# Performance work log

Hardware: AMD Instinct MI355X
Metric: run time of the kernel (lower is better)

## Reference

```python
import jax, jax.numpy as jnp
import numpy as np

H, L, P, D_MODEL = 8, 4, 4, 256
HD = D_MODEL // H
SPATIAL = np.array([[100, 100], [50, 50], [25, 25], [13, 13]], dtype=np.int64)  # (h, w) per level


def _bilinear_sample(feat, gx, gy, lh, lw):
    """Bilinear sampling matching torch.F.grid_sample(align_corners=False, padding_mode='zeros').
    feat: [BH, lh*lw, D]; gx, gy: [BH, Nq, P] pixel coords. Returns [BH, Nq, P, D]."""
    x0 = jnp.floor(gx); y0 = jnp.floor(gy)
    wx = gx - x0; wy = gy - y0

    def gather(xf, yf):
        xi = xf.astype(jnp.int32); yi = yf.astype(jnp.int32)
        valid = (xi >= 0) & (xi < lw) & (yi >= 0) & (yi < lh)
        idx = jnp.clip(yi, 0, lh - 1) * lw + jnp.clip(xi, 0, lw - 1)
        BH = feat.shape[0]
        v = jnp.take_along_axis(feat, idx.reshape(BH, -1)[:, :, None], axis=1)
        v = v.reshape(xi.shape + (feat.shape[-1],))
        return v * valid[..., None].astype(feat.dtype)

    return (gather(x0, y0) * ((1 - wx) * (1 - wy))[..., None]
            + gather(x0 + 1, y0) * (wx * (1 - wy))[..., None]
            + gather(x0, y0 + 1) * ((1 - wx) * wy)[..., None]
            + gather(x0 + 1, y0 + 1) * (wx * wy)[..., None])


def _msda(query, reference_points, value, sp_np, Wso, bso, Waw, baw, Wv, bv, Wo, bo):
    B, Nq, _ = query.shape
    Nv = value.shape[1]
    v = (value @ Wv + bv).reshape(B, Nv, H, HD)  # value_proj
    off = (query @ Wso + bso).reshape(B, Nq, H, L, P, 2)  # sampling_offsets
    wh = jnp.asarray(sp_np[:, ::-1].copy(), jnp.float32)  # (w, h) per level
    loc = reference_points[:, :, None, :, None, :] + off / wh[None, None, None, :, None, :]
    grid = 2.0 * loc - 1.0  # [B, Nq, H, L, P, 2] in [-1, 1]
    aw = jax.nn.softmax((query @ Waw + baw).reshape(B, Nq, H, L * P), axis=-1).reshape(B, Nq, H, L, P)
    starts = np.concatenate([[0], np.cumsum(sp_np[:, 0] * sp_np[:, 1])]).astype(np.int64)
    out = jnp.zeros((B, H, Nq, HD), dtype=query.dtype)
    for lid in range(L):
        lh, lw = int(sp_np[lid, 0]), int(sp_np[lid, 1])
        feat = v[:, starts[lid]:starts[lid + 1]].transpose(0, 2, 1, 3).reshape(B * H, lh * lw, HD)
        g = grid[:, :, :, lid].transpose(0, 2, 1, 3, 4).reshape(B * H, Nq, P, 2)
        # align_corners=False: x_pix = ((gx + 1) * W - 1) / 2
        gx = (g[..., 0] + 1.0) * (lw * 0.5) - 0.5
        gy = (g[..., 1] + 1.0) * (lh * 0.5) - 0.5
        samp = _bilinear_sample(feat, gx, gy, lh, lw)  # [B*H, Nq, P, HD]
        w_l = aw[:, :, :, lid].transpose(0, 2, 1, 3).reshape(B * H, Nq, P)
        out = out + (samp * w_l[..., None]).sum(axis=2).reshape(B, H, Nq, HD)
    out = out.transpose(0, 2, 1, 3).reshape(B, Nq, D_MODEL)
    return out @ Wo + bo  # output_proj


def setup_inputs() -> dict:
    key = jax.random.key(0)
    ks = jax.random.split(key, 12)
    B, Nq = 2, int(np.sum(SPATIAL[:, 0] * SPATIAL[:, 1]))  # encoder: Nq == Nv == 13294
    Nv = Nq
    s = 1.0 / np.sqrt(D_MODEL).astype(np.float32)
    return {
        "query": jax.random.normal(ks[0], (B, Nq, D_MODEL), jnp.float32),
        "reference_points": jax.random.uniform(ks[1], (B, Nq, L, 2), dtype=jnp.float32),
        "value": jax.random.normal(ks[2], (B, Nv, D_MODEL), jnp.float32),
        "spatial_shapes": jnp.asarray(SPATIAL),
        "Wso": jax.random.normal(ks[3], (D_MODEL, H * L * P * 2), jnp.float32) * 0.01,
        "bso": jax.random.normal(ks[4], (H * L * P * 2,), jnp.float32) * 0.5,
        "Waw": jax.random.normal(ks[5], (D_MODEL, H * L * P), jnp.float32) * 0.01,
        "baw": jnp.zeros((H * L * P,), jnp.float32),
        "Wv": jax.random.normal(ks[6], (D_MODEL, D_MODEL), jnp.float32) * s,
        "bv": jnp.zeros((D_MODEL,), jnp.float32),
        "Wo": jax.random.normal(ks[7], (D_MODEL, D_MODEL), jnp.float32) * s,
        "bo": jnp.zeros((D_MODEL,), jnp.float32),
    }


def reference(query, reference_points, value, spatial_shapes, Wso, bso, Waw, baw, Wv, bv, Wo, bo):
    sp_np = np.asarray(spatial_shapes)  # static level shapes
    return _msda(query, reference_points, value, sp_np, Wso, bso, Waw, baw, Wv, bv, Wo, bo)
```

## Files before the change

### kernel.cpp

```cpp
#include <hip/hip_runtime.h>
#include <hip/hip_bf16.h>
#include <hip/hip_fp16.h>

typedef short s16x8 __attribute__((ext_vector_type(8)));
typedef float f32x4 __attribute__((ext_vector_type(4)));
typedef unsigned int u32x4 __attribute__((ext_vector_type(4)));
typedef unsigned int u32x2 __attribute__((ext_vector_type(2)));

constexpr int Bb = 2, NQ = 13294, Hh = 8, HD = 32;
constexpr int Mrows = Bb * NQ;

__device__ inline short bf16_of(float f) {
  __hip_bfloat16 h = __float2bfloat16(f);
  return *reinterpret_cast<short*>(&h);
}

__device__ __forceinline__ void gload16(const void* g, void* l) {
  __builtin_amdgcn_global_load_lds(
      (const __attribute__((address_space(1))) unsigned int*)g,
      (__attribute__((address_space(3))) unsigned int*)l, 16, 0, 0);
}

__global__ __launch_bounds__(256) void prep_k(
    const float* __restrict__ Wv, const float* __restrict__ Wso,
    const float* __restrict__ Waw, const float* __restrict__ Wo,
    const float* __restrict__ bso, const float* __restrict__ baw,
    short* __restrict__ WvT, short* __restrict__ WqT, short* __restrict__ WoT,
    float* __restrict__ bq)
{
  __shared__ short lds[64][65];
  const int tid = threadIdx.x;
  int t = blockIdx.x;
  if (t == 56) {
#pragma unroll
    for (int i = 0; i < 2; i++) {
      int id = i * 256 + tid;
      if (id < 384) bq[id] = id < 256 ? bso[id] : baw[id - 256];
    }
    return;
  }
  const float* src; short* dst; int ldS, n0, k0, drow0;
  if (t < 16)      { src = Wv;  dst = WvT; ldS = 256; n0 = (t >> 2) * 64;        k0 = (t & 3) * 64; drow0 = n0; }
  else if (t < 32) { t -= 16; src = Wso; dst = WqT; ldS = 256; n0 = (t >> 2) * 64; k0 = (t & 3) * 64; drow0 = n0; }
  else if (t < 40) { t -= 32; src = Waw; dst = WqT; ldS = 128; n0 = (t >> 2) * 64; k0 = (t & 3) * 64; drow0 = 256 + n0; }
  else             { t -= 40; src = Wo;  dst = WoT; ldS = 256; n0 = (t >> 2) * 64; k0 = (t & 3) * 64; drow0 = n0; }

#pragma unroll
  for (int i = 0; i < 16; i++) {
    int idx = i * 256 + tid;
    int kk = idx >> 6, nn = idx & 63;
    lds[nn][kk] = bf16_of(src[(size_t)(k0 + kk) * ldS + n0 + nn]);
  }
  __syncthreads();
#pragma unroll
  for (int i = 0; i < 16; i++) {
    int idx = i * 256 + tid;
    int nn = idx >> 6, kk = idx & 63;
    dst[(size_t)(drow0 + nn) * 256 + k0 + kk] = lds[nn][kk];
  }
}

template<int MODE>
__device__ __forceinline__ void gemm_body(
    const void* __restrict__ Araw, const short* __restrict__ WT,
    const float* __restrict__ bias, void* __restrict__ outraw,
    int wg, char* __restrict__ ldsA, char* __restrict__ ldsB)
{
  constexpr int NT = (MODE == 1) ? 6 : 4;
  constexpr int ABYTES = (MODE == 3) ? 8192 : 16384;
  const int xcd = wg & 7, local = wg >> 3;
  const int row0 = (xcd * 26 + local / NT) * 128;
  const int col0 = (local % NT) * 64;
  const int tid = threadIdx.x, lane = tid & 63, wave = tid >> 6;
  const int fr = lane & 15, kg = lane >> 4;

  float bvf[4];
#pragma unroll
  for (int n = 0; n < 4; n++) bvf[n] = bias[col0 + n * 16 + fr];
  asm volatile("" :: "v"(bvf[0]), "v"(bvf[1]), "v"(bvf[2]), "v"(bvf[3]));

  const int rowB = tid >> 2, slB = (tid & 3) ^ (rowB & 3);
  const short* srcB = WT + (size_t)(col0 + rowB) * 256 + slB * 8;
  const int ldoffB = tid * 16;

  const float* srcAf[4]; const short* srcAs[2]; int ldoffA[4];
  if constexpr (MODE == 3) {
#pragma unroll
    for (int i = 0; i < 2; i++) {
      int rowA = i * 64 + (tid >> 2);
      int rowc = min(row0 + rowA, Mrows - 1);
      int slA = (tid & 3) ^ (rowA & 3);
      srcAs[i] = (const short*)Araw + (size_t)rowc * 256 + slA * 8;
      ldoffA[i] = i * 4096 + tid * 16;
    }
  } else {
#pragma unroll
    for (int i = 0; i < 4; i++) {
      int rowA = i * 32 + (tid >> 3);
      int rowc = min(row0 + rowA, Mrows - 1);
      int slA = (tid & 7) ^ (rowA & 7);
      srcAf[i] = (const float*)Araw + (size_t)rowc * 256 + slA * 4;
      ldoffA[i] = i * 4096 + tid * 16;
    }
  }

  auto stage = [&](int bufsel, int kt) {
    char* Ab = ldsA + bufsel * ABYTES;
    char* Bd = ldsB + bufsel * 4096;
    if constexpr (MODE == 3) {
#pragma unroll
      for (int i = 0; i < 2; i++) gload16(srcAs[i] + kt, Ab + ldoffA[i]);
    } else {
#pragma unroll
      for (int i = 0; i < 4; i++) gload16(srcAf[i] + kt, Ab + ldoffA[i]);
    }
    gload16(srcB + kt, Bd + ldoffB);
  };

  f32x4 acc[2][4] = {};
  stage(0, 0);

#pragma unroll
  for (int t = 0; t < 8; t++) {
    const int buf = t & 1;
    if (t < 7) {
      stage(buf ^ 1, (t + 1) * 32);
      if constexpr (MODE == 3) asm volatile("s_waitcnt vmcnt(3)" ::: "memory");
      else                     asm volatile("s_waitcnt vmcnt(5)" ::: "memory");
    } else {
      asm volatile("s_waitcnt vmcnt(0)" ::: "memory");
    }
    __builtin_amdgcn_s_barrier();

    const char* Ab = ldsA + buf * ABYTES;
    const char* Bd = ldsB + buf * 4096;
    s16x8 afr[2], bfr[4];
#pragma unroll
    for (int m = 0; m < 2; m++) {
      const int row = wave * 32 + m * 16 + fr;
      if constexpr (MODE == 3) {
        const int slot = kg ^ (row & 3);
        afr[m] = *(const s16x8*)(Ab + row * 64 + slot * 16);
      } else {
        const int s0 = (2 * kg) ^ (row & 7);
        const f32x4 lo = *(const f32x4*)(Ab + row * 128 + s0 * 16);
        const f32x4 hi = *(const f32x4*)(Ab + row * 128 + (s0 ^ 1) * 16);
        s16x8 av;
#pragma unroll
        for (int i = 0; i < 4; i++) { av[i] = bf16_of(lo[i]); av[4 + i] = bf16_of(hi[i]); }
        afr[m] = av;
      }
    }
#pragma unroll
    for (int n = 0; n < 4; n++) {
      const int row = n * 16 + fr;
      const int slot = kg ^ (row & 3);
      bfr[n] = *(const s16x8*)(Bd + row * 64 + slot * 16);
    }
    asm volatile("s_waitcnt lgkmcnt(0)" ::: "memory");
    __builtin_amdgcn_s_barrier();

#pragma unroll
    for (int m = 0; m < 2; m++)
#pragma unroll
      for (int n = 0; n < 4; n++)
        acc[m][n] = __builtin_amdgcn_mfma_f32_16x16x32_bf16(afr[m], bfr[n], acc[m][n], 0, 0, 0);
  }

#pragma unroll
  for (int n = 0; n < 4; n++) {
    const int colL = col0 + n * 16 + fr;
#pragma unroll
    for (int m = 0; m < 2; m++) {
#pragma unroll
      for (int r = 0; r < 4; r++) {
        const int rowL = row0 + wave * 32 + m * 16 + kg * 4 + r;
        if (rowL < Mrows) {
          float v = acc[m][n][r] + bvf[n];
          if constexpr (MODE == 0) {
            int b = rowL >= NQ, nn = rowL - b * NQ;
            int h = colL >> 5, c = colL & 31;
            ((__half*)outraw)[(((size_t)b * Hh + h) * NQ + nn) * HD + c] = __float2half(v);
          } else if constexpr (MODE == 1) {
            ((__hip_bfloat16*)outraw)[(size_t)rowL * 384 + colL] = __float2bfloat16(v);
          } else {
            ((float*)outraw)[(size_t)rowL * 256 + colL] = v;
          }
        }
      }
    }
  }
}

__global__ __launch_bounds__(256) void gemm01_k(
    const float* __restrict__ value, const float* __restrict__ query,
    const short* __restrict__ WvT, const short* __restrict__ WqT,
    const float* __restrict__ bv, const float* __restrict__ bq,
    __half* __restrict__ vproj, __hip_bfloat16* __restrict__ offaw)
{
  __shared__ __align__(16) char lds[40960];
  char* ldsA = lds;
  char* ldsB = lds + 32768;
  const int wg = blockIdx.x;
  if (wg < 832) gemm_body<0>(value, WvT, bv, vproj, wg, ldsA, ldsB);
  else          gemm_body<1>(query, WqT, bq, offaw, wg - 832, ldsA, ldsB);
}

__global__ __launch_bounds__(256) void gemm3_k(
    const short* __restrict__ interm, const short* __restrict__ WoT,
    const float* __restrict__ bo, float* __restrict__ out)
{
  __shared__ __align__(16) char lds[24576];
  char* ldsA = lds;
  char* ldsB = lds + 16384;
  gemm_body<3>(interm, WoT, bo, out, blockIdx.x, ldsA, ldsB);
}

__global__ __launch_bounds__(256, 8) void sample_k(
    const __half* __restrict__ vproj,
    const __hip_bfloat16* __restrict__ offaw,
    const float* __restrict__ refp,
    __hip_bfloat16* __restrict__ interm)
{
  __shared__ u32x2 dpk[16][2][65];
  const int plane = blockIdx.x & 15;
  const int chunk = blockIdx.x >> 4;
  const int b = plane >> 3, h = plane & 7;
  const int q0 = chunk * 64;
  const int tid = threadIdx.x;
  const int wv = tid >> 6, lane = tid & 63;
  const int dims[4]   = {100, 50, 25, 13};
  const int starts[4] = {0, 10000, 12500, 13125};

#pragma unroll
  for (int it = 0; it < 4; it++) {
    const int ql = wv * 16 + it * 4 + (lane >> 4);
    const int lp = lane & 15;
    const int l = lp >> 2;
    const int lw = dims[l];
    int q = q0 + ql; if (q >= NQ) q = NQ - 1;
    const size_t row = (size_t)b * NQ + q;
    unsigned int oxy = *(const unsigned int*)((const unsigned short*)offaw + row * 384 + h * 32 + lp * 2);
    float offx = __uint_as_float(oxy << 16);
    float offy = __uint_as_float(oxy & 0xffff0000u);
    float logit = __bfloat162float(offaw[row * 384 + 256 + h * 16 + lp]);
    float2 rp = *(const float2*)(refp + (row * 4 + l) * 2);
    float gx = rp.x * (float)lw + offx - 0.5f;
    float gy = rp.y * (float)lw + offy - 0.5f;
    float e = __expf(logit);
    float ssum = e;
#pragma unroll
    for (int d = 1; d < 16; d <<= 1) ssum += __shfl_xor(ssum, d);
    float aw = e / ssum;

    float xf = floorf(gx), yf = floorf(gy);
    int x0 = (int)xf, y0 = (int)yf;
    float wx = gx - xf, wy = gy - yf;
    int bx = min(max(x0, 0), lw - 2);
    bool lxv = (x0 >= 0) & (x0 < lw);
    bool rxv = (x0 + 1 >= 0) & (x0 + 1 < lw);
    float wl = 1.f - wx, wr = wx;
    float ws0 = (lxv && x0 == bx     ? wl : 0.f) + (rxv && x0 + 1 == bx     ? wr : 0.f);
    float ws1 = (lxv && x0 == bx + 1 ? wl : 0.f) + (rxv && x0 + 1 == bx + 1 ? wr : 0.f);
    const int pbase = (b * Hh + h) * NQ + starts[l];
#pragma unroll
    for (int yi = 0; yi < 2; yi++) {
      int yc = y0 + yi;
      bool yv = (yc >= 0) & (yc < lw);
      int ycl = min(max(yc, 0), lw - 1);
      float wyt = (yi ? wy : 1.f - wy) * aw * (yv ? 1.f : 0.f);
      __half h0 = __float2half(ws0 * wyt);
      __half h1 = __float2half(ws1 * wyt);
      u32x2 pk;
      pk[0] = (unsigned int)((pbase + ycl * lw + bx) << 6);
      pk[1] = (unsigned int)(*(unsigned short*)&h0)
            | ((unsigned int)(*(unsigned short*)&h1) << 16);
      dpk[lp][yi][ql] = pk;
    }
  }
  asm volatile("s_waitcnt lgkmcnt(0)" ::: "memory");

  const int qh8 = lane >> 3;
  const int c8  = lane & 7;
  const int shsel = (c8 & 4) << 2;
  const int coff = c8 * 16;
#pragma unroll
  for (int half = 0; half < 2; half++) {
    const int ql = wv * 16 + half * 8 + qh8;
    __half2 acc2[4] = {};
#pragma unroll 4
    for (int lp = 0; lp < 16; lp++) {
#pragma unroll
      for (int yi = 0; yi < 2; yi++) {
        const u32x2 d = dpk[lp][yi][ql];
        const u32x4 u = *(const u32x4*)((const char*)vproj + d[0] + coff);
        unsigned short hw = (unsigned short)((d[1] >> shsel) & 0xffffu);
        __half2 ww = __half2half2(*(const __half*)&hw);
#pragma unroll
        for (int j = 0; j < 4; j++) {
          unsigned int t0 = u[j];
          acc2[j] = __hfma2(*reinterpret_cast<__half2*>(&t0), ww, acc2[j]);
        }
      }
    }
    float2 f[4];
#pragma unroll
    for (int j = 0; j < 4; j++) {
      f[j] = __half22float2(acc2[j]);
      f[j].x += __shfl_xor(f[j].x, 4);
      f[j].y += __shfl_xor(f[j].y, 4);
    }
    const int q = q0 + ql;
    if (c8 < 4 && q < NQ) {
      unsigned int up[4];
#pragma unroll
      for (int j = 0; j < 4; j++) {
        unsigned int b0 = (unsigned int)(unsigned short)bf16_of(f[j].x);
        unsigned int b1 = (unsigned int)(unsigned short)bf16_of(f[j].y);
        up[j] = (b1 << 16) | b0;
      }
      u32x4 pk = { up[0], up[1], up[2], up[3] };
      *(u32x4*)((unsigned short*)interm + ((size_t)b * NQ + q) * 256 + h * 32 + c8 * 8) = pk;
    }
  }
}

extern "C" void kernel_launch(void* const* d_in, const int* in_sizes, int n_in,
                              void* d_out, int out_size, void* d_ws, size_t ws_size,
                              hipStream_t stream)
{
  const float* query = (const float*)d_in[0];
  const float* refp  = (const float*)d_in[1];
  const float* value = (const float*)d_in[2];
  const float* Wso = (const float*)d_in[4];
  const float* bso = (const float*)d_in[5];
  const float* Waw = (const float*)d_in[6];
  const float* baw = (const float*)d_in[7];
  const float* Wv  = (const float*)d_in[8];
  const float* bv  = (const float*)d_in[9];
  const float* Wo  = (const float*)d_in[10];
  const float* bo  = (const float*)d_in[11];

  char* ws = (char*)d_ws;
  __half* vproj          = (__half*)ws;
  __hip_bfloat16* offaw  = (__hip_bfloat16*)(ws + 13613056);
  __hip_bfloat16* interm = (__hip_bfloat16*)(ws + 34032640);
  short* WvT = (short*)(ws + 47645696);
  short* WqT = (short*)(ws + 47776768);
  short* WoT = (short*)(ws + 47973376);
  float* bq  = (float*)(ws + 48104448);
  float* out = (float*)d_out;

  dim3 blk(256);
  prep_k<<<dim3(57), blk, 0, stream>>>(Wv, Wso, Waw, Wo, bso, baw, WvT, WqT, WoT, bq);
  gemm01_k<<<dim3(832 + 1248), blk, 0, stream>>>(value, query, WvT, WqT, bv, bq, vproj, offaw);
  sample_k<<<dim3(16 * 208), blk, 0, stream>>>(vproj, offaw, refp, interm);
  gemm3_k<<<dim3(832), blk, 0, stream>>>((const short*)interm, WoT, bo, out);
}
```

Baseline: 80.90 us.

## Widen GEMM tiles to 128x128 with 2x2 wave layout

Switches the GEMM body from 128x64 output tiles (each wave owning 32 rows by 64 columns) to 128x128 tiles on a 2x2 wave grid, each wave computing 64x64 with a 4x4 MFMA accumulator array. B staging doubles to two global-to-LDS loads per stage, the LDS swizzle moves to a (row>>1)&3 pattern, and the workgroup counts for both GEMM launches are halved. The goal is more reuse of A, so the fp32 activations are loaded and converted to bf16 fewer times, but it raises register and LDS use per workgroup and leaves fewer workgroups to fill the CUs.

```diff
diff --git a/kernel.cpp b/kernel.cpp
--- a/kernel.cpp
+++ b/kernel.cpp
@@ -66,30 +66,35 @@
     const float* __restrict__ bias, void* __restrict__ outraw,
     int wg, char* __restrict__ ldsA, char* __restrict__ ldsB)
 {
-  constexpr int NT = (MODE == 1) ? 6 : 4;
+  constexpr int NT = (MODE == 1) ? 3 : 2;
   constexpr int ABYTES = (MODE == 3) ? 8192 : 16384;
   const int xcd = wg & 7, local = wg >> 3;
   const int row0 = (xcd * 26 + local / NT) * 128;
-  const int col0 = (local % NT) * 64;
+  const int col0 = (local % NT) * 128;
   const int tid = threadIdx.x, lane = tid & 63, wave = tid >> 6;
+  const int wr = (wave >> 1) * 64, wc = (wave & 1) * 64;
   const int fr = lane & 15, kg = lane >> 4;
 
   float bvf[4];
 #pragma unroll
-  for (int n = 0; n < 4; n++) bvf[n] = bias[col0 + n * 16 + fr];
+  for (int n = 0; n < 4; n++) bvf[n] = bias[col0 + wc + n * 16 + fr];
   asm volatile("" :: "v"(bvf[0]), "v"(bvf[1]), "v"(bvf[2]), "v"(bvf[3]));
 
-  const int rowB = tid >> 2, slB = (tid & 3) ^ (rowB & 3);
-  const short* srcB = WT + (size_t)(col0 + rowB) * 256 + slB * 8;
-  const int ldoffB = tid * 16;
-
+  const short* srcB[2]; int ldoffB[2];
+#pragma unroll
+  for (int i = 0; i < 2; i++) {
+    int rowB = i * 64 + (tid >> 2);
+    int slB = (tid & 3) ^ ((rowB >> 1) & 3);
+    srcB[i] = WT + (size_t)(col0 + rowB) * 256 + slB * 8;
+    ldoffB[i] = i * 4096 + tid * 16;
+  }
   const float* srcAf[4]; const short* srcAs[2]; int ldoffA[4];
   if constexpr (MODE == 3) {
 #pragma unroll
     for (int i = 0; i < 2; i++) {
       int rowA = i * 64 + (tid >> 2);
       int rowc = min(row0 + rowA, Mrows - 1);
-      int slA = (tid & 3) ^ (rowA & 3);
+      int slA = (tid & 3) ^ ((rowA >> 1) & 3);
       srcAs[i] = (const short*)Araw + (size_t)rowc * 256 + slA * 8;
       ldoffA[i] = i * 4096 + tid * 16;
     }
@@ -106,7 +111,7 @@
 
   auto stage = [&](int bufsel, int kt) {
     char* Ab = ldsA + bufsel * ABYTES;
-    char* Bd = ldsB + bufsel * 4096;
+    char* Bd = ldsB + bufsel * 8192;
     if constexpr (MODE == 3) {
 #pragma unroll
       for (int i = 0; i < 2; i++) gload16(srcAs[i] + kt, Ab + ldoffA[i]);
@@ -114,10 +119,11 @@
 #pragma unroll
       for (int i = 0; i < 4; i++) gload16(srcAf[i] + kt, Ab + ldoffA[i]);
     }
-    gload16(srcB + kt, Bd + ldoffB);
+#pragma unroll
+    for (int i = 0; i < 2; i++) gload16(srcB[i] + kt, Bd + ldoffB[i]);
   };
 
-  f32x4 acc[2][4] = {};
+  f32x4 acc[4][4] = {};
   stage(0, 0);
 
 #pragma unroll
@@ -125,21 +131,21 @@
     const int buf = t & 1;
     if (t < 7) {
       stage(buf ^ 1, (t + 1) * 32);
-      if constexpr (MODE == 3) asm volatile("s_waitcnt vmcnt(3)" ::: "memory");
-      else                     asm volatile("s_waitcnt vmcnt(5)" ::: "memory");
+      if constexpr (MODE == 3) asm volatile("s_waitcnt vmcnt(4)" ::: "memory");
+      else                     asm volatile("s_waitcnt vmcnt(6)" ::: "memory");
     } else {
       asm volatile("s_waitcnt vmcnt(0)" ::: "memory");
     }
     __builtin_amdgcn_s_barrier();
 
     const char* Ab = ldsA + buf * ABYTES;
-    const char* Bd = ldsB + buf * 4096;
-    s16x8 afr[2], bfr[4];
-#pragma unroll
-    for (int m = 0; m < 2; m++) {
-      const int row = wave * 32 + m * 16 + fr;
+    const char* Bd = ldsB + buf * 8192;
+    s16x8 afr[4], bfr[4];
+#pragma unroll
+    for (int m = 0; m < 4; m++) {
+      const int row = wr + m * 16 + fr;
       if constexpr (MODE == 3) {
-        const int slot = kg ^ (row & 3);
+        const int slot = kg ^ ((row >> 1) & 3);
         afr[m] = *(const s16x8*)(Ab + row * 64 + slot * 16);
       } else {
         const int s0 = (2 * kg) ^ (row & 7);
@@ -153,15 +159,15 @@
     }
 #pragma unroll
     for (int n = 0; n < 4; n++) {
-      const int row = n * 16 + fr;
-      const int slot = kg ^ (row & 3);
+      const int row = wc + n * 16 + fr;
+      const int slot = kg ^ ((row >> 1) & 3);
       bfr[n] = *(const s16x8*)(Bd + row * 64 + slot * 16);
     }
     asm volatile("s_waitcnt lgkmcnt(0)" ::: "memory");
     __builtin_amdgcn_s_barrier();
 
 #pragma unroll
-    for (int m = 0; m < 2; m++)
+    for (int m = 0; m < 4; m++)
 #pragma unroll
       for (int n = 0; n < 4; n++)
         acc[m][n] = __builtin_amdgcn_mfma_f32_16x16x32_bf16(afr[m], bfr[n], acc[m][n], 0, 0, 0);
@@ -169,12 +175,12 @@
 
 #pragma unroll
   for (int n = 0; n < 4; n++) {
-    const int colL = col0 + n * 16 + fr;
-#pragma unroll
-    for (int m = 0; m < 2; m++) {
+    const int colL = col0 + wc + n * 16 + fr;
+#pragma unroll
+    for (int m = 0; m < 4; m++) {
 #pragma unroll
       for (int r = 0; r < 4; r++) {
-        const int rowL = row0 + wave * 32 + m * 16 + kg * 4 + r;
+        const int rowL = row0 + wr + m * 16 + kg * 4 + r;
         if (rowL < Mrows) {
           float v = acc[m][n][r] + bvf[n];
           if constexpr (MODE == 0) {
@@ -198,19 +204,19 @@
     const float* __restrict__ bv, const float* __restrict__ bq,
     __half* __restrict__ vproj, __hip_bfloat16* __restrict__ offaw)
 {
-  __shared__ __align__(16) char lds[40960];
+  __shared__ __align__(16) char lds[49152];
   char* ldsA = lds;
   char* ldsB = lds + 32768;
   const int wg = blockIdx.x;
-  if (wg < 832) gemm_body<0>(value, WvT, bv, vproj, wg, ldsA, ldsB);
-  else          gemm_body<1>(query, WqT, bq, offaw, wg - 832, ldsA, ldsB);
+  if (wg < 416) gemm_body<0>(value, WvT, bv, vproj, wg, ldsA, ldsB);
+  else          gemm_body<1>(query, WqT, bq, offaw, wg - 416, ldsA, ldsB);
 }
 
 __global__ __launch_bounds__(256) void gemm3_k(
     const short* __restrict__ interm, const short* __restrict__ WoT,
     const float* __restrict__ bo, float* __restrict__ out)
 {
-  __shared__ __align__(16) char lds[24576];
+  __shared__ __align__(16) char lds[32768];
   char* ldsA = lds;
   char* ldsB = lds + 16384;
   gemm_body<3>(interm, WoT, bo, out, blockIdx.x, ldsA, ldsB);
@@ -353,7 +359,7 @@
 
   dim3 blk(256);
   prep_k<<<dim3(57), blk, 0, stream>>>(Wv, Wso, Waw, Wo, bso, baw, WvT, WqT, WoT, bq);
-  gemm01_k<<<dim3(832 + 1248), blk, 0, stream>>>(value, query, WvT, WqT, bv, bq, vproj, offaw);
+  gemm01_k<<<dim3(416 + 624), blk, 0, stream>>>(value, query, WvT, WqT, bv, bq, vproj, offaw);
   sample_k<<<dim3(16 * 208), blk, 0, stream>>>(vproj, offaw, refp, interm);
-  gemm3_k<<<dim3(832), blk, 0, stream>>>((const short*)interm, WoT, bo, out);
-}
+  gemm3_k<<<dim3(416), blk, 0, stream>>>((const short*)interm, WoT, bo, out);
+}
```

Result: no change. 79.77 us (-1.4%).
